# Kernel optimization log

Measured on AMD Instinct MI355X. Metric: run time of the kernel, lower is better.

Reference implementation:

```python
import jax, jax.numpy as jnp
import numpy as np

# model dims (match init_kwargs)
EMBED_DIM = 1024
NUM_HEADS = 16
HEAD_DIM = EMBED_DIM // NUM_HEADS  # 64
WS = 256           # window_size[0]*window_size[1] = 16*16
NW = 64            # number of windows
M = NW * WS        # gathered length = 16384
L = M - 1          # raw tokens (padding row appended makes M rows)
SCALE = HEAD_DIM ** -0.5


def _rope(t, cos, sin):
    # t: [M, H, d]; cos/sin: [M, d] -> broadcast over heads
    c = cos[:, None, :]
    s = sin[:, None, :]
    half = HEAD_DIM // 2
    rot = jnp.concatenate([-t[..., half:], t[..., :half]], axis=-1)
    return t * c + rot * s


def setup_inputs() -> dict:
    key = jax.random.key(0)
    ks = jax.random.split(key, 8)
    x = jax.random.normal(ks[0], (L, EMBED_DIM), jnp.float32)
    # kv_indices: permutation of all M rows (incl. padding row index L) so every
    # token lands in exactly one window slot, as the scatter-back assumes.
    kv_indices = jax.random.permutation(ks[1], M).astype(jnp.int64)
    q_indices = kv_indices            # unused in the manual (non-xformers) branch
    inv_indices = jnp.arange(L, dtype=jnp.int64)  # unused in the manual branch
    # rotary tables over gathered positions
    pos = jnp.arange(M, dtype=jnp.float32)
    inv_freq = 1.0 / (10000.0 ** (jnp.arange(0, HEAD_DIM, 2, dtype=jnp.float32) / HEAD_DIM))
    ang = pos[:, None] * inv_freq[None, :]          # [M, d/2]
    ang = jnp.concatenate([ang, ang], axis=-1)      # [M, d]
    rope_cos = jnp.cos(ang)
    rope_sin = jnp.sin(ang)
    # learned params
    qkv_w = jax.random.normal(ks[2], (3 * EMBED_DIM, EMBED_DIM), jnp.float32) * (EMBED_DIM ** -0.5)
    qkv_b = jax.random.normal(ks[3], (3 * EMBED_DIM,), jnp.float32) * 0.02
    proj_w = jax.random.normal(ks[4], (EMBED_DIM, EMBED_DIM), jnp.float32) * (EMBED_DIM ** -0.5)
    proj_b = jax.random.normal(ks[5], (EMBED_DIM,), jnp.float32) * 0.02
    padding = jnp.zeros((1, EMBED_DIM), jnp.float32)  # nn.Parameter(torch.zeros(1, D))
    return {"x": x, "qkv_w": qkv_w, "qkv_b": qkv_b, "proj_w": proj_w,
            "proj_b": proj_b, "padding": padding, "rope_cos": rope_cos,
            "rope_sin": rope_sin, "kv_indices": kv_indices,
            "q_indices": q_indices, "inv_indices": inv_indices, "ws": WS}


def reference(x, qkv_w, qkv_b, proj_w, proj_b, padding, rope_cos, rope_sin,
              kv_indices, q_indices, inv_indices, ws):
    # append padding row: [L+1, D]
    xp = jnp.concatenate([x, padding], axis=0)
    # fused qkv projection -> [M, 3, H, d]
    qkv = (xp @ qkv_w.T + qkv_b).reshape(-1, 3, NUM_HEADS, HEAD_DIM)
    q, k, v = qkv[:, 0], qkv[:, 1], qkv[:, 2]
    # manual windowed branch: gather q/k/v with kv_indices, RoPE (mode='key') on q and k
    qg = _rope(q[kv_indices], rope_cos, rope_sin)   # [M, H, d]
    kg = _rope(k[kv_indices], rope_cos, rope_sin)
    vg = v[kv_indices]
    nw = M // ws
    qw = qg.reshape(nw, ws, NUM_HEADS, HEAD_DIM)
    kw = kg.reshape(nw, ws, NUM_HEADS, HEAD_DIM)
    vw = vg.reshape(nw, ws, NUM_HEADS, HEAD_DIM)
    attn = jax.nn.softmax(SCALE * jnp.einsum('wind,wjnd->wnij', qw, kw), axis=-1)
    ow = jnp.einsum('wnij,wjnd->wind', attn, vw).reshape(M, NUM_HEADS * HEAD_DIM)
    # scatter back to original token order, drop padding row
    ori = jnp.zeros((M, EMBED_DIM), x.dtype).at[kv_indices].set(ow)
    out = ori[:L] @ proj_w.T + proj_b
    return out
```

## Files before the change

kernel.cpp:

```cpp
#include <hip/hip_runtime.h>
#include <hip/hip_bf16.h>

#define EMBED 1024
#define THREE_EMBED 3072
#define NHEAD 16
#define HDIM 64
#define MTOT 16384
#define LTOT 16383

typedef __attribute__((ext_vector_type(8))) short bf16x8;
typedef __attribute__((ext_vector_type(4))) float f32x4;

__device__ __forceinline__ unsigned short f2b(float f) {
  union { float f; unsigned u; } v; v.f = f;
  unsigned r = v.u + 0x7fffu + ((v.u >> 16) & 1u);
  return (unsigned short)(r >> 16);
}
__device__ __forceinline__ float b2f(unsigned short h) {
  union { unsigned u; float f; } v; v.u = ((unsigned)h) << 16;
  return v.f;
}

__device__ __forceinline__ void gload16(const void* g, void* l) {
  __builtin_amdgcn_global_load_lds(
      (const __attribute__((address_space(1))) void*)g,
      (__attribute__((address_space(3))) void*)l, 16, 0, 0);
}

#define BARRIER() asm volatile("s_barrier" ::: "memory")

__global__ __launch_bounds__(256) void cast_inputs(
    const float* __restrict__ x, const float* __restrict__ padding,
    const float* __restrict__ wq, const float* __restrict__ wp,
    const int* __restrict__ kvi,
    unsigned short* __restrict__ xb, unsigned short* __restrict__ wqb,
    unsigned short* __restrict__ wpb, int* __restrict__ inv, int np)
{
  const int NX = MTOT * EMBED / 8;
  const int NQ = THREE_EMBED * EMBED / 8;
  const int total = NX + NQ + np;
  int g = blockIdx.x * 256 + threadIdx.x;
  const int stride = gridDim.x * 256;
  for (; g < total + MTOT; g += stride) {
    if (g >= total) {
      int i = g - total;
      inv[kvi[i]] = i;
      continue;
    }
    const float* src;
    unsigned short* dst;
    if (g < NX) {
      size_t e = (size_t)g * 8;
      int row = (int)(e >> 10);
      src = (row < LTOT) ? (x + e) : (padding + (e - (size_t)LTOT * 1024));
      dst = xb + e;
    } else if (g < NX + NQ) {
      size_t e = (size_t)(g - NX) * 8;
      src = wq + e;
      dst = wqb + e;
    } else {
      size_t e = (size_t)(g - NX - NQ) * 8;
      src = wp + e;
      dst = wpb + e;
    }
    float4 a = *(const float4*)src;
    float4 b = *(const float4*)(src + 4);
    ushort4 u0, u1;
    u0.x = f2b(a.x); u0.y = f2b(a.y); u0.z = f2b(a.z); u0.w = f2b(a.w);
    u1.x = f2b(b.x); u1.y = f2b(b.y); u1.z = f2b(b.z); u1.w = f2b(b.w);
    *(ushort4*)dst = u0;
    *(ushort4*)(dst + 4) = u1;
  }
}

template <int EPI>
__global__ __launch_bounds__(512, 2) void gemm256(
    const unsigned short* __restrict__ A, const unsigned short* __restrict__ B,
    const float* __restrict__ bias, const int* __restrict__ idx,
    unsigned short* __restrict__ outb, float* __restrict__ outf)
{
  __shared__ __align__(16) unsigned short lds[65536];
  const int t = threadIdx.x;
  const int lane = t & 63, wid = t >> 6;
  const int l15 = lane & 15, quad = lane >> 4;
  const int wr = wid >> 2, wc = wid & 3;
  const int bm = blockIdx.x, bn = blockIdx.y;

  const int srow = wid * 8 + (lane >> 3);
  const int scol = ((lane & 7) ^ (lane >> 3)) * 8;
  const unsigned short* gA = A + (size_t)(bm * 256 + srow) * EMBED + scol;
  const unsigned short* gB = B + (size_t)(bn * 256 + srow) * EMBED + scol;

  auto stA = [&](int p, int R0, int kt) {
    const unsigned short* g = gA + (size_t)R0 * EMBED + kt * 64;
    char* d = (char*)lds + p * 32768 + R0 * 128 + wid * 1024;
    gload16(g, d);
    gload16(g + (size_t)64 * EMBED, d + 8192);
  };
  auto stB = [&](int p, int R0, int kt) {
    const unsigned short* g = gB + (size_t)R0 * EMBED + kt * 64;
    char* d = (char*)lds + 65536 + p * 32768 + R0 * 128 + wid * 1024;
    gload16(g, d);
    gload16(g + (size_t)64 * EMBED, d + 8192);
  };

  const int aOff = (wr * 128 + l15) * 64;
  const int bOff = (wc * 64 + l15) * 64;
  const int swz0 = (quad ^ (l15 & 7)) * 8;
  const int swz1 = ((quad + 4) ^ (l15 & 7)) * 8;

  f32x4 acc[8][4];
#pragma unroll
  for (int i = 0; i < 8; ++i)
#pragma unroll
    for (int j = 0; j < 4; ++j) acc[i][j] = (f32x4){0.f, 0.f, 0.f, 0.f};

  stA(0, 0, 0); stA(0, 128, 0); stB(0, 0, 0); stB(0, 128, 0);
  stB(1, 0, 1); stB(1, 128, 1);
  asm volatile("s_waitcnt vmcnt(4)" ::: "memory");
  BARRIER();

#define MFMAGRP(MB)                                                          \
  _Pragma("unroll") for (int m = 0; m < 4; ++m)                              \
      _Pragma("unroll") for (int n = 0; n < 4; ++n)                          \
          acc[(MB) + m][n] = __builtin_amdgcn_mfma_f32_16x16x32_bf16(        \
              a[m], b[n], acc[(MB) + m][n], 0, 0, 0);

#define TILE(P, KT, STA, STB, WCNT)                                          \
  {                                                                          \
    const unsigned short* Ab = lds + (P) * 16384 + aOff;                     \
    const unsigned short* Bb = lds + 32768 + (P) * 16384 + bOff;             \
    bf16x8 a[4], b[4];                                                       \
    {                                               \
      _Pragma("unroll") for (int n = 0; n < 4; ++n)                          \
          b[n] = *(const bf16x8*)(Bb + n * 1024 + swz0);                     \
      _Pragma("unroll") for (int m = 0; m < 4; ++m)                          \
          a[m] = *(const bf16x8*)(Ab + m * 1024 + swz0);                     \
      if (STA) stA((P) ^ 1, 0, (KT) + 1);                                    \
      BARRIER();                                                             \
      __builtin_amdgcn_s_setprio(1);                                         \
      MFMAGRP(0);                                                            \
      __builtin_amdgcn_s_setprio(0);                                         \
      BARRIER();                                                             \
    }                                                                        \
    {                                               \
      _Pragma("unroll") for (int m = 0; m < 4; ++m)                          \
          a[m] = *(const bf16x8*)(Ab + (4 + m) * 1024 + swz0);               \
      if (STA) stA((P) ^ 1, 128, (KT) + 1);                                  \
      BARRIER();                                                             \
      __builtin_amdgcn_s_setprio(1);                                         \
      MFMAGRP(4);                                                            \
      __builtin_amdgcn_s_setprio(0);                                         \
      BARRIER();                                                             \
    }                                                                        \
    {                                               \
      _Pragma("unroll") for (int n = 0; n < 4; ++n)                          \
          b[n] = *(const bf16x8*)(Bb + n * 1024 + swz1);                     \
      _Pragma("unroll") for (int m = 0; m < 4; ++m)                          \
          a[m] = *(const bf16x8*)(Ab + m * 1024 + swz1);                     \
      if (STB) stB((P), 0, (KT) + 2);                                        \
      BARRIER();                                                             \
      __builtin_amdgcn_s_setprio(1);                                         \
      MFMAGRP(0);                                                            \
      __builtin_amdgcn_s_setprio(0);                                         \
      BARRIER();                                                             \
    }                                                                        \
    {                                               \
      _Pragma("unroll") for (int m = 0; m < 4; ++m)                          \
          a[m] = *(const bf16x8*)(Ab + (4 + m) * 1024 + swz1);               \
      if (STB) stB((P), 128, (KT) + 2);                                      \
      BARRIER();                                                             \
      __builtin_amdgcn_s_setprio(1);                                         \
      MFMAGRP(4);                                                            \
      __builtin_amdgcn_s_setprio(0);                                         \
      if ((WCNT) == 4) asm volatile("s_waitcnt vmcnt(4)" ::: "memory");      \
      if ((WCNT) == 0) asm volatile("s_waitcnt vmcnt(0)" ::: "memory");      \
      BARRIER();                                                             \
    }                                                                        \
  }

#pragma unroll 1
  for (int t2 = 0; t2 < 7; ++t2) {
    const int kt = t2 * 2;
    TILE(0, kt, 1, 1, 4);
    TILE(1, kt + 1, 1, 1, 4);
  }
  TILE(0, 14, 1, 0, 0);
  TILE(1, 15, 0, 0, -1);
#undef TILE
#undef MFMAGRP

  float bv[4];
#pragma unroll
  for (int nt = 0; nt < 4; ++nt)
    bv[nt] = bias[bn * 256 + wc * 64 + nt * 16 + l15];
  if constexpr (EPI == 0) {
    const int hh = bn * 4 + wc;
    unsigned short* buf = outb + (size_t)hh * (MTOT * HDIM);
#pragma unroll
    for (int mt = 0; mt < 8; ++mt) {
#pragma unroll
      for (int reg = 0; reg < 4; ++reg) {
        int row = bm * 256 + wr * 128 + mt * 16 + quad * 4 + reg;
        int i = idx[row];
#pragma unroll
        for (int nt = 0; nt < 4; ++nt)
          buf[(size_t)i * HDIM + nt * 16 + l15] =
              f2b(acc[mt][nt][reg] + bv[nt]);
      }
    }
  } else {
    const int col = bn * 256 + wc * 64;
#pragma unroll
    for (int mt = 0; mt < 8; ++mt) {
#pragma unroll
      for (int reg = 0; reg < 4; ++reg) {
        int i = bm * 256 + wr * 128 + mt * 16 + quad * 4 + reg;
        int orow = idx[i];
        if (orow < LTOT) {
#pragma unroll
          for (int nt = 0; nt < 4; ++nt)
            outf[(size_t)orow * EMBED + col + nt * 16 + l15] =
                acc[mt][nt][reg] + bv[nt];
        }
      }
    }
  }
}

__global__ __launch_bounds__(256) void cast_w(
    const float* __restrict__ w, unsigned short* __restrict__ wb)
{
  int g = blockIdx.x * 256 + threadIdx.x;
  size_t e = (size_t)g * 8;
  float4 a = *(const float4*)(w + e);
  float4 b = *(const float4*)(w + e + 4);
  ushort4 u0, u1;
  u0.x = f2b(a.x); u0.y = f2b(a.y); u0.z = f2b(a.z); u0.w = f2b(a.w);
  u1.x = f2b(b.x); u1.y = f2b(b.y); u1.z = f2b(b.z); u1.w = f2b(b.w);
  *(ushort4*)(wb + e) = u0;
  *(ushort4*)(wb + e + 4) = u1;
}

__global__ __launch_bounds__(256, 3) void attn(
    const unsigned short* __restrict__ qkvh,
    const float* __restrict__ rope_cos, const float* __restrict__ rope_sin,
    unsigned short* __restrict__ ow)
{
  __shared__ __align__(16) unsigned short sK[128 * 64];
  __shared__ __align__(16) unsigned short sV[64 * 128];
  __shared__ __align__(16) unsigned short sP[4][16 * 40];

  const int t = threadIdx.x;
  const int lane = t & 63, wid = t >> 6;
  const int l15 = lane & 15, quad = lane >> 4;
  const int wwin = blockIdx.x >> 4;
  const int h = blockIdx.x & 15;

  const unsigned short* Qh = qkvh + (size_t)h * (MTOT * HDIM);
  const unsigned short* Kh = qkvh + (size_t)(16 + h) * (MTOT * HDIM);
  const unsigned short* Vh = qkvh + (size_t)(32 + h) * (MTOT * HDIM);

  f32x4 accO[4][4];
  float mrow[4][4], lrow[4][4];
#pragma unroll
  for (int qt = 0; qt < 4; ++qt) {
#pragma unroll
    for (int nt = 0; nt < 4; ++nt) accO[qt][nt] = (f32x4){0.f, 0.f, 0.f, 0.f};
#pragma unroll
    for (int reg = 0; reg < 4; ++reg) { mrow[qt][reg] = -1e30f; lrow[qt][reg] = 0.f; }
  }

  bf16x8 qa[4][2];
#pragma unroll
  for (int qt = 0; qt < 4; ++qt) {
    int i = wwin * 256 + wid * 64 + qt * 16 + l15;
    const unsigned short* qp = Qh + (size_t)i * HDIM;
    const float* cp = rope_cos + (size_t)i * HDIM + quad * 8;
    const float* sp = rope_sin + (size_t)i * HDIM + quad * 8;
    bf16x8 qlo = *(const bf16x8*)(qp + quad * 8);
    bf16x8 qhi = *(const bf16x8*)(qp + 32 + quad * 8);
    float cl[8], ch[8], sl[8], sh[8];
    *(float4*)(cl)     = *(const float4*)(cp);
    *(float4*)(cl + 4) = *(const float4*)(cp + 4);
    *(float4*)(ch)     = *(const float4*)(cp + 32);
    *(float4*)(ch + 4) = *(const float4*)(cp + 36);
    *(float4*)(sl)     = *(const float4*)(sp);
    *(float4*)(sl + 4) = *(const float4*)(sp + 4);
    *(float4*)(sh)     = *(const float4*)(sp + 32);
    *(float4*)(sh + 4) = *(const float4*)(sp + 36);
#pragma unroll
    for (int j = 0; j < 8; ++j) {
      float a = b2f((unsigned short)qlo[j]);
      float b = b2f((unsigned short)qhi[j]);
      qa[qt][0][j] = (short)f2b((a * cl[j] - b * sl[j]) * 0.125f);
      qa[qt][1][j] = (short)f2b((b * ch[j] + a * sh[j]) * 0.125f);
    }
  }

  for (int half = 0; half < 2; ++half) {
    __syncthreads();
    {
      int key = t >> 1, hx = t & 1;
      int i = wwin * 256 + half * 128 + key;
      int k7 = key & 7;
      const unsigned short* kp = Kh + (size_t)i * HDIM;
      const float* cp = rope_cos + (size_t)i * HDIM;
      const float* sp = rope_sin + (size_t)i * HDIM;
#pragma unroll
      for (int cc = 0; cc < 2; ++cc) {
        int dlo = hx * 16 + cc * 8;
        int dhi = dlo + 32;
        bf16x8 klo = *(const bf16x8*)(kp + dlo);
        bf16x8 khi = *(const bf16x8*)(kp + dhi);
        float cl[8], ch[8], sl[8], sh[8];
        *(float4*)(cl)     = *(const float4*)(cp + dlo);
        *(float4*)(cl + 4) = *(const float4*)(cp + dlo + 4);
        *(float4*)(ch)     = *(const float4*)(cp + dhi);
        *(float4*)(ch + 4) = *(const float4*)(cp + dhi + 4);
        *(float4*)(sl)     = *(const float4*)(sp + dlo);
        *(float4*)(sl + 4) = *(const float4*)(sp + dlo + 4);
        *(float4*)(sh)     = *(const float4*)(sp + dhi);
        *(float4*)(sh + 4) = *(const float4*)(sp + dhi + 4);
        bf16x8 olo, ohi;
#pragma unroll
        for (int j = 0; j < 8; ++j) {
          float a = b2f((unsigned short)klo[j]);
          float b = b2f((unsigned short)khi[j]);
          olo[j] = (short)f2b(a * cl[j] - b * sl[j]);
          ohi[j] = (short)f2b(b * ch[j] + a * sh[j]);
        }
        int clo = dlo >> 3;
        int chi = dhi >> 3;
        *(uint4*)(sK + key * 64 + ((clo ^ k7) * 8)) = *(uint4*)&olo;
        *(uint4*)(sK + key * 64 + ((chi ^ k7) * 8)) = *(uint4*)&ohi;
      }
      const unsigned short* vp = Vh + (size_t)i * HDIM + hx * 32;
      int kc3 = key >> 3;
#pragma unroll
      for (int c = 0; c < 4; ++c) {
        bf16x8 va = *(const bf16x8*)(vp + c * 8);
#pragma unroll
        for (int j = 0; j < 8; ++j) {
          int d = hx * 32 + c * 8 + j;
          sV[d * 128 + ((kc3 ^ (d & 7)) * 8) + (key & 7)] =
              (unsigned short)va[j];
        }
      }
    }
    __syncthreads();

#pragma unroll
    for (int qt = 0; qt < 4; ++qt) {
      f32x4 accS[8];
#pragma unroll
      for (int nt = 0; nt < 8; ++nt) accS[nt] = (f32x4){0.f, 0.f, 0.f, 0.f};
#pragma unroll
      for (int ks = 0; ks < 2; ++ks) {
#pragma unroll
        for (int nt = 0; nt < 8; ++nt) {
          int key = nt * 16 + l15;
          bf16x8 bk = *(const bf16x8*)(
              sK + key * 64 + (((ks * 4 + quad) ^ (key & 7)) * 8));
          accS[nt] = __builtin_amdgcn_mfma_f32_16x16x32_bf16(
              qa[qt][ks], bk, accS[nt], 0, 0, 0);
        }
      }
#pragma unroll
      for (int reg = 0; reg < 4; ++reg) {
        float mx = accS[0][reg];
#pragma unroll
        for (int nt = 1; nt < 8; ++nt) mx = fmaxf(mx, accS[nt][reg]);
#pragma unroll
        for (int off = 1; off < 16; off <<= 1)
          mx = fmaxf(mx, __shfl_xor(mx, off, 64));
        float mold = mrow[qt][reg];
        float mnew = fmaxf(mold, mx);
        float alpha = __expf(mold - mnew);
        mrow[qt][reg] = mnew;
        float ls = 0.f;
#pragma unroll
        for (int nt = 0; nt < 8; ++nt) {
          float p = __expf(accS[nt][reg] - mnew);
          accS[nt][reg] = p;
          ls += p;
        }
#pragma unroll
        for (int off = 1; off < 16; off <<= 1) ls += __shfl_xor(ls, off, 64);
        lrow[qt][reg] = lrow[qt][reg] * alpha + ls;
#pragma unroll
        for (int nt = 0; nt < 4; ++nt) accO[qt][nt][reg] *= alpha;
      }
#pragma unroll
      for (int kc = 0; kc < 4; ++kc) {
#pragma unroll
        for (int nt2 = 0; nt2 < 2; ++nt2) {
#pragma unroll
          for (int reg = 0; reg < 4; ++reg) {
            sP[wid][(quad * 4 + reg) * 40 + nt2 * 16 + l15] =
                f2b(accS[kc * 2 + nt2][reg]);
          }
        }
        bf16x8 pa = *(const bf16x8*)(&sP[wid][l15 * 40 + quad * 8]);
#pragma unroll
        for (int nt = 0; nt < 4; ++nt) {
          int d = nt * 16 + l15;
          bf16x8 bv = *(const bf16x8*)(
              sV + d * 128 + (((kc * 4 + quad) ^ (d & 7)) * 8));
          accO[qt][nt] = __builtin_amdgcn_mfma_f32_16x16x32_bf16(
              pa, bv, accO[qt][nt], 0, 0, 0);
        }
      }
    }
  }

  __syncthreads();
  unsigned short* scr = sK + wid * 2048;
  const int rlane = lane >> 3;
  const int clane = (lane & 7) * 8;
#pragma unroll
  for (int qt = 0; qt < 4; ++qt) {
#pragma unroll
    for (int reg = 0; reg < 4; ++reg) {
      float invl = 1.0f / lrow[qt][reg];
      int r = quad * 4 + reg;
#pragma unroll
      for (int nt = 0; nt < 4; ++nt)
        scr[r * 72 + nt * 16 + l15] = f2b(accO[qt][nt][reg] * invl);
    }
#pragma unroll
    for (int rr = 0; rr < 2; ++rr) {
      int row = rr * 8 + rlane;
      bf16x8 vv = *(const bf16x8*)(scr + row * 72 + clane);
      int i = wwin * 256 + wid * 64 + qt * 16 + row;
      *(bf16x8*)(ow + (size_t)i * EMBED + h * HDIM + clane) = vv;
    }
  }
}

extern "C" void kernel_launch(void* const* d_in, const int* in_sizes, int n_in,
                              void* d_out, int out_size, void* d_ws, size_t ws_size,
                              hipStream_t stream) {
  const float* x        = (const float*)d_in[0];
  const float* qkv_w    = (const float*)d_in[1];
  const float* qkv_b    = (const float*)d_in[2];
  const float* proj_w   = (const float*)d_in[3];
  const float* proj_b   = (const float*)d_in[4];
  const float* padding  = (const float*)d_in[5];
  const float* rope_cos = (const float*)d_in[6];
  const float* rope_sin = (const float*)d_in[7];
  const int*   kvi      = (const int*)d_in[8];

  const size_t QKVH_B = (size_t)MTOT * THREE_EMBED * 2;
  const size_t R_B    = (size_t)MTOT * EMBED * 2;
  const size_t W_B    = (size_t)EMBED * EMBED * 2;
  unsigned short* qkvh = (unsigned short*)d_ws;
  unsigned short* R    = (unsigned short*)((char*)d_ws + QKVH_B);
  unsigned short* xb = R;
  unsigned short* ow = R;
  unsigned short* wqb = (unsigned short*)d_out;
  const bool roomy = ws_size >= QKVH_B + R_B + W_B;
  unsigned short* wpb = roomy
      ? (unsigned short*)((char*)d_ws + QKVH_B + R_B)
      : qkvh;
  int* inv = (int*)((char*)d_out + (size_t)LTOT * EMBED * 4 - (size_t)MTOT * 4);
  float* out = (float*)d_out;

  cast_inputs<<<4096, 256, 0, stream>>>(
      x, padding, qkv_w, roomy ? proj_w : nullptr, kvi, xb, wqb, wpb, inv,
      roomy ? (EMBED * EMBED / 8) : 0);
  gemm256<0><<<dim3(64, 12), 512, 0, stream>>>(xb, wqb, qkv_b, inv, qkvh,
                                               nullptr);
  attn<<<dim3(64 * 16), 256, 0, stream>>>(qkvh, rope_cos, rope_sin, ow);
  if (!roomy) cast_w<<<512, 256, 0, stream>>>(proj_w, wpb);
  gemm256<1><<<dim3(64, 4), 512, 0, stream>>>(ow, wpb, proj_b, kvi, nullptr,
                                              out);
}
```

Measured before the change: 408.0 us.

## Split RoPE into standalone kernel and double-buffer K/V staging in attention

Moves the RoPE rotation (and the Q scale) for Q and K out of the attention kernel into a separate in-place elementwise pass over the qkv buffer. This lets the attention kernel stage K with async global-to-LDS loads and prefetch V into registers, using double-buffered K/V shared memory so the second half's loads overlap the first half's compute. The cost is an extra kernel launch plus a full read and write of the Q/K data, and a lower occupancy hint (2 blocks per CU instead of 3) to make room for the doubled LDS.

```diff
diff --git a/kernel.cpp b/kernel.cpp
--- a/kernel.cpp
+++ b/kernel.cpp
@@ -228,6 +228,41 @@
   }
 }
 
+__global__ __launch_bounds__(256) void rope_qk(
+    const float* __restrict__ rope_cos, const float* __restrict__ rope_sin,
+    unsigned short* __restrict__ qkvh)
+{
+  int g = blockIdx.x * 256 + threadIdx.x;
+  int dc = g & 3;
+  int i  = (g >> 2) & (MTOT - 1);
+  int hh = g >> 16;
+  unsigned short* p = qkvh + ((size_t)hh * MTOT + i) * HDIM;
+  bf16x8 lo = *(const bf16x8*)(p + dc * 8);
+  bf16x8 hi = *(const bf16x8*)(p + 32 + dc * 8);
+  const float* cp = rope_cos + (size_t)i * HDIM + dc * 8;
+  const float* sp = rope_sin + (size_t)i * HDIM + dc * 8;
+  float cl[8], ch[8], sl[8], sh[8];
+  *(float4*)(cl)     = *(const float4*)(cp);
+  *(float4*)(cl + 4) = *(const float4*)(cp + 4);
+  *(float4*)(ch)     = *(const float4*)(cp + 32);
+  *(float4*)(ch + 4) = *(const float4*)(cp + 36);
+  *(float4*)(sl)     = *(const float4*)(sp);
+  *(float4*)(sl + 4) = *(const float4*)(sp + 4);
+  *(float4*)(sh)     = *(const float4*)(sp + 32);
+  *(float4*)(sh + 4) = *(const float4*)(sp + 36);
+  const float sc = (hh < 16) ? 0.125f : 1.0f;
+  bf16x8 olo, ohi;
+#pragma unroll
+  for (int j = 0; j < 8; ++j) {
+    float a = b2f((unsigned short)lo[j]);
+    float b = b2f((unsigned short)hi[j]);
+    olo[j] = (short)f2b((a * cl[j] - b * sl[j]) * sc);
+    ohi[j] = (short)f2b((b * ch[j] + a * sh[j]) * sc);
+  }
+  *(bf16x8*)(p + dc * 8) = olo;
+  *(bf16x8*)(p + 32 + dc * 8) = ohi;
+}
+
 __global__ __launch_bounds__(256) void cast_w(
     const float* __restrict__ w, unsigned short* __restrict__ wb)
 {
@@ -242,13 +277,12 @@
   *(ushort4*)(wb + e + 4) = u1;
 }
 
-__global__ __launch_bounds__(256, 3) void attn(
+__global__ __launch_bounds__(256, 2) void attn(
     const unsigned short* __restrict__ qkvh,
-    const float* __restrict__ rope_cos, const float* __restrict__ rope_sin,
     unsigned short* __restrict__ ow)
 {
-  __shared__ __align__(16) unsigned short sK[128 * 64];
-  __shared__ __align__(16) unsigned short sV[64 * 128];
+  __shared__ __align__(16) unsigned short sK[2][128 * 64];
+  __shared__ __align__(16) unsigned short sV[2][64 * 128];
   __shared__ __align__(16) unsigned short sP[4][16 * 40];
 
   const int t = threadIdx.x;
@@ -261,6 +295,31 @@
   const unsigned short* Kh = qkvh + (size_t)(16 + h) * (MTOT * HDIM);
   const unsigned short* Vh = qkvh + (size_t)(32 + h) * (MTOT * HDIM);
 
+  const int l3 = lane >> 3, l7 = lane & 7;
+  const unsigned short* ksrc =
+      Kh + (size_t)(wwin * 256 + wid * 32 + l3) * HDIM + (l7 ^ l3) * 8;
+  auto stageK = [&](int buf, int half) {
+#pragma unroll
+    for (int p = 0; p < 4; ++p)
+      gload16(ksrc + (size_t)(half * 128 + p * 8) * HDIM,
+              (char*)&sK[buf][(wid * 32 + p * 8) * 64]);
+  };
+
+  const int vkey = t >> 1, vhx = t & 1;
+  const unsigned short* vsrc =
+      Vh + (size_t)(wwin * 256 + vkey) * HDIM + vhx * 32;
+  auto writeV = [&](int buf, bf16x8* vr) {
+    int kc3 = vkey >> 3, k7 = vkey & 7;
+#pragma unroll
+    for (int c = 0; c < 4; ++c)
+#pragma unroll
+      for (int j = 0; j < 8; ++j) {
+        int d = vhx * 32 + c * 8 + j;
+        sV[buf][d * 128 + ((kc3 ^ (d & 7)) * 8) + k7] =
+            (unsigned short)vr[c][j];
+      }
+  };
+
   f32x4 accO[4][4];
   float mrow[4][4], lrow[4][4];
 #pragma unroll
@@ -271,85 +330,27 @@
     for (int reg = 0; reg < 4; ++reg) { mrow[qt][reg] = -1e30f; lrow[qt][reg] = 0.f; }
   }
 
+  stageK(0, 0);
+  bf16x8 vr0[4], vr1[4];
+#pragma unroll
+  for (int c = 0; c < 4; ++c) vr0[c] = *(const bf16x8*)(vsrc + c * 8);
   bf16x8 qa[4][2];
 #pragma unroll
   for (int qt = 0; qt < 4; ++qt) {
     int i = wwin * 256 + wid * 64 + qt * 16 + l15;
     const unsigned short* qp = Qh + (size_t)i * HDIM;
-    const float* cp = rope_cos + (size_t)i * HDIM + quad * 8;
-    const float* sp = rope_sin + (size_t)i * HDIM + quad * 8;
-    bf16x8 qlo = *(const bf16x8*)(qp + quad * 8);
-    bf16x8 qhi = *(const bf16x8*)(qp + 32 + quad * 8);
-    float cl[8], ch[8], sl[8], sh[8];
-    *(float4*)(cl)     = *(const float4*)(cp);
-    *(float4*)(cl + 4) = *(const float4*)(cp + 4);
-    *(float4*)(ch)     = *(const float4*)(cp + 32);
-    *(float4*)(ch + 4) = *(const float4*)(cp + 36);
-    *(float4*)(sl)     = *(const float4*)(sp);
-    *(float4*)(sl + 4) = *(const float4*)(sp + 4);
-    *(float4*)(sh)     = *(const float4*)(sp + 32);
-    *(float4*)(sh + 4) = *(const float4*)(sp + 36);
-#pragma unroll
-    for (int j = 0; j < 8; ++j) {
-      float a = b2f((unsigned short)qlo[j]);
-      float b = b2f((unsigned short)qhi[j]);
-      qa[qt][0][j] = (short)f2b((a * cl[j] - b * sl[j]) * 0.125f);
-      qa[qt][1][j] = (short)f2b((b * ch[j] + a * sh[j]) * 0.125f);
-    }
-  }
-
-  for (int half = 0; half < 2; ++half) {
-    __syncthreads();
-    {
-      int key = t >> 1, hx = t & 1;
-      int i = wwin * 256 + half * 128 + key;
-      int k7 = key & 7;
-      const unsigned short* kp = Kh + (size_t)i * HDIM;
-      const float* cp = rope_cos + (size_t)i * HDIM;
-      const float* sp = rope_sin + (size_t)i * HDIM;
-#pragma unroll
-      for (int cc = 0; cc < 2; ++cc) {
-        int dlo = hx * 16 + cc * 8;
-        int dhi = dlo + 32;
-        bf16x8 klo = *(const bf16x8*)(kp + dlo);
-        bf16x8 khi = *(const bf16x8*)(kp + dhi);
-        float cl[8], ch[8], sl[8], sh[8];
-        *(float4*)(cl)     = *(const float4*)(cp + dlo);
-        *(float4*)(cl + 4) = *(const float4*)(cp + dlo + 4);
-        *(float4*)(ch)     = *(const float4*)(cp + dhi);
-        *(float4*)(ch + 4) = *(const float4*)(cp + dhi + 4);
-        *(float4*)(sl)     = *(const float4*)(sp + dlo);
-        *(float4*)(sl + 4) = *(const float4*)(sp + dlo + 4);
-        *(float4*)(sh)     = *(const float4*)(sp + dhi);
-        *(float4*)(sh + 4) = *(const float4*)(sp + dhi + 4);
-        bf16x8 olo, ohi;
-#pragma unroll
-        for (int j = 0; j < 8; ++j) {
-          float a = b2f((unsigned short)klo[j]);
-          float b = b2f((unsigned short)khi[j]);
-          olo[j] = (short)f2b(a * cl[j] - b * sl[j]);
-          ohi[j] = (short)f2b(b * ch[j] + a * sh[j]);
-        }
-        int clo = dlo >> 3;
-        int chi = dhi >> 3;
-        *(uint4*)(sK + key * 64 + ((clo ^ k7) * 8)) = *(uint4*)&olo;
-        *(uint4*)(sK + key * 64 + ((chi ^ k7) * 8)) = *(uint4*)&ohi;
-      }
-      const unsigned short* vp = Vh + (size_t)i * HDIM + hx * 32;
-      int kc3 = key >> 3;
-#pragma unroll
-      for (int c = 0; c < 4; ++c) {
-        bf16x8 va = *(const bf16x8*)(vp + c * 8);
-#pragma unroll
-        for (int j = 0; j < 8; ++j) {
-          int d = hx * 32 + c * 8 + j;
-          sV[d * 128 + ((kc3 ^ (d & 7)) * 8) + (key & 7)] =
-              (unsigned short)va[j];
-        }
-      }
-    }
-    __syncthreads();
-
+    qa[qt][0] = *(const bf16x8*)(qp + quad * 8);
+    qa[qt][1] = *(const bf16x8*)(qp + 32 + quad * 8);
+  }
+  asm volatile("s_waitcnt vmcnt(0)" ::: "memory");
+  writeV(0, vr0);
+  stageK(1, 1);
+#pragma unroll
+  for (int c = 0; c < 4; ++c)
+    vr1[c] = *(const bf16x8*)(vsrc + (size_t)128 * HDIM + c * 8);
+  __syncthreads();
+
+  auto compute = [&](const unsigned short* sKb, const unsigned short* sVb) {
 #pragma unroll
     for (int qt = 0; qt < 4; ++qt) {
       f32x4 accS[8];
@@ -361,7 +362,7 @@
         for (int nt = 0; nt < 8; ++nt) {
           int key = nt * 16 + l15;
           bf16x8 bk = *(const bf16x8*)(
-              sK + key * 64 + (((ks * 4 + quad) ^ (key & 7)) * 8));
+              sKb + key * 64 + (((ks * 4 + quad) ^ (key & 7)) * 8));
           accS[nt] = __builtin_amdgcn_mfma_f32_16x16x32_bf16(
               qa[qt][ks], bk, accS[nt], 0, 0, 0);
         }
@@ -406,16 +407,23 @@
         for (int nt = 0; nt < 4; ++nt) {
           int d = nt * 16 + l15;
           bf16x8 bv = *(const bf16x8*)(
-              sV + d * 128 + (((kc * 4 + quad) ^ (d & 7)) * 8));
+              sVb + d * 128 + (((kc * 4 + quad) ^ (d & 7)) * 8));
           accO[qt][nt] = __builtin_amdgcn_mfma_f32_16x16x32_bf16(
               pa, bv, accO[qt][nt], 0, 0, 0);
         }
       }
     }
-  }
-
+  };
+
+  compute(&sK[0][0], &sV[0][0]);
+  asm volatile("s_waitcnt vmcnt(0)" ::: "memory");
   __syncthreads();
-  unsigned short* scr = sK + wid * 2048;
+  writeV(1, vr1);
+  __syncthreads();
+  compute(&sK[1][0], &sV[1][0]);
+
+  __syncthreads();
+  unsigned short* scr = &sK[0][0] + wid * 2048;
   const int rlane = lane >> 3;
   const int clane = (lane & 7) * 8;
 #pragma unroll
@@ -471,7 +479,8 @@
       roomy ? (EMBED * EMBED / 8) : 0);
   gemm256<0><<<dim3(64, 12), 512, 0, stream>>>(xb, wqb, qkv_b, inv, qkvh,
                                                nullptr);
-  attn<<<dim3(64 * 16), 256, 0, stream>>>(qkvh, rope_cos, rope_sin, ow);
+  rope_qk<<<8192, 256, 0, stream>>>(rope_cos, rope_sin, qkvh);
+  attn<<<dim3(64 * 16), 256, 0, stream>>>(qkvh, ow);
   if (!roomy) cast_w<<<512, 256, 0, stream>>>(proj_w, wpb);
   gemm256<1><<<dim3(64, 4), 512, 0, stream>>>(ow, wpb, proj_b, kvi, nullptr,
                                               out);
```

Measured after the change: 366.3 us. -10.2%, faster.
